# Kernel tuning notes

Hardware: AMD Instinct MI355X
Metric: run time of the kernel (lower is better)

The kernel has to match this reference:

```python
import jax, jax.numpy as jnp
import numpy as np

N = 30000   # fluid particles
E = 480000  # edges
F = 4       # fluidFeatures (in channels)
P = 8       # RBF basis size per dim (dims=[8], 1D)
LAYERS = [32, 64, 64, 2]


def hat_basis(x, n):
    # 'linear' RBF: hat functions on n evenly spaced centers in [-1, 1]
    centers = jnp.linspace(-1.0, 1.0, n, dtype=x.dtype)
    spacing = 2.0 / (n - 1)
    return jnp.maximum(0.0, 1.0 - jnp.abs(x[:, None] - centers[None, :]) / spacing)  # [E, n]


def rbf_conv(x, fi, fj, d, W, b, mask, n_nodes):
    # x: [N, Cin]; d: [E, 1] clamped; W: [P, Cin, Cout]; b: [Cout]
    phi = hat_basis(d[:, 0], W.shape[0])      # [E, P]
    xj = x[fj]                                 # gather source features [E, Cin]
    msg = jnp.zeros((xj.shape[0], W.shape[2]), dtype=x.dtype)
    for p in range(W.shape[0]):                # small fixed P=8 loop keeps memory O(E*Cout)
        msg = msg + phi[:, p, None] * (xj @ W[p])
    msg = jnp.where(mask[:, None], msg, 0.0)   # centerIgnore: drop self edges fi==fj
    out = jax.ops.segment_sum(msg, fi, num_segments=n_nodes)  # scatter-reduce to targets
    return out + b


def _xavier(key, shape_in, shape_out):
    lim = float(np.sqrt(6.0 / (shape_in + shape_out)))
    return jax.random.uniform(key, (shape_in, shape_out), jnp.float32, -lim, lim)


def setup_inputs() -> dict:
    key = jax.random.key(0)
    ks = jax.random.split(key, 16)
    fluidFeatures = jax.random.normal(ks[0], (N, F), jnp.float32)
    fi = jax.random.randint(ks[1], (E,), 0, N)
    fj = jax.random.randint(ks[2], (E,), 0, N)
    distances = jax.random.normal(ks[3], (E, 1), jnp.float32)
    # conv channels: 4->32, 64->64, 64->64, 64->2
    cio = [(F, 32), (2 * 32, 64), (64, 64), (64, 2)]
    inp = {"fluidFeatures": fluidFeatures, "fi": fi, "fj": fj, "distances": distances}
    for li, (ci, co) in enumerate(cio):
        inp[f"cW{li}"] = jax.random.normal(ks[4 + li], (P, ci, co), jnp.float32) * (1.0 / np.sqrt(P * ci))
        inp[f"cb{li}"] = jnp.zeros((co,), jnp.float32)
        inp[f"fW{li}"] = _xavier(ks[8 + li], ci, co)   # stored [in, out]
        inp[f"fb{li}"] = jnp.zeros((co,), jnp.float32)
    return inp


def reference(fluidFeatures, fi, fj, distances,
              cW0, cb0, fW0, fb0, cW1, cb1, fW1, fb1,
              cW2, cb2, fW2, fb2, cW3, cb3, fW3, fb3):
    n_nodes = fluidFeatures.shape[0]
    mask = fi != fj                     # centerIgnore (mask instead of filter: jit-safe)
    d = jnp.clip(distances, -1.0, 1.0)

    conv0 = rbf_conv(fluidFeatures, fi, fj, d, cW0, cb0, mask, n_nodes)  # [N, 32]
    lin0 = fluidFeatures @ fW0 + fb0                                      # [N, 32]
    ans = jnp.concatenate([lin0, conv0], axis=1)                          # [N, 64]

    # i = 1: features[0]=32 != features[1]=64 -> no residual
    ansc = jax.nn.relu(ans)
    ans = rbf_conv(ansc, fi, fj, d, cW1, cb1, mask, n_nodes) + (ansc @ fW1 + fb1)
    # i = 2: features[1]==features[2]==64 and shapes match -> residual
    ansc = jax.nn.relu(ans)
    ans = rbf_conv(ansc, fi, fj, d, cW2, cb2, mask, n_nodes) + (ansc @ fW2 + fb2) + ans
    # i = 3: 64 -> 2, no residual
    ansc = jax.nn.relu(ans)
    ans = rbf_conv(ansc, fi, fj, d, cW3, cb3, mask, n_nodes) + (ansc @ fW3 + fb3)

    return ans  # dim == 1 (dims=[8]) -> no /128
```

## Files before the change

kernel.cpp:

```cpp
#include <hip/hip_runtime.h>


#define CAP 48

typedef __attribute__((ext_vector_type(8))) short short8;
typedef __attribute__((ext_vector_type(4))) float f32x4;
typedef int v4i __attribute__((ext_vector_type(4)));

__device__ __forceinline__ short bf16s(float f) {
  unsigned u = __float_as_uint(f);
  return (short)((u + 0x7FFF + ((u >> 16) & 1)) >> 16);
}
__device__ __forceinline__ float b2f(unsigned short s) {
  return __uint_as_float(((unsigned)s) << 16);
}
__device__ __forceinline__ unsigned pack2(float a, float b) {
  return (unsigned)(unsigned short)bf16s(a) | ((unsigned)(unsigned short)bf16s(b) << 16);
}
__device__ __forceinline__ float dec_w0(int v) {
  return __uint_as_float(0x3F800000u | (((unsigned)v & 0xFFFu) << 11)) - 1.0f;
}
__device__ __forceinline__ float dec_sf(int v) {
  return (float)(((unsigned)v >> 12) & 1u);
}
__device__ __forceinline__ unsigned long long rfl64(unsigned long long x) {
  unsigned lo = __builtin_amdgcn_readfirstlane((unsigned)x);
  unsigned hi = __builtin_amdgcn_readfirstlane((unsigned)(x >> 32));
  return ((unsigned long long)hi << 32) | (unsigned long long)lo;
}

#define LOAD_RECS32Q(JROW, CPTR, MRAW)                                      \
  v4i q0, q1, q2, q3, q4, q5, q6, q7;                                       \
  int MRAW;                                                                 \
  asm volatile("s_load_dwordx4 %0, %9, 0x0\n\t"                             \
               "s_load_dwordx4 %1, %9, 0x10\n\t"                            \
               "s_load_dwordx4 %2, %9, 0x20\n\t"                            \
               "s_load_dwordx4 %3, %9, 0x30\n\t"                            \
               "s_load_dwordx4 %4, %9, 0x40\n\t"                            \
               "s_load_dwordx4 %5, %9, 0x50\n\t"                            \
               "s_load_dwordx4 %6, %9, 0x60\n\t"                            \
               "s_load_dwordx4 %7, %9, 0x70\n\t"                            \
               "s_load_dword %8, %10, 0x0\n\t"                              \
               "s_waitcnt lgkmcnt(0)"                                       \
               : "=&s"(q0), "=&s"(q1), "=&s"(q2), "=&s"(q3), "=&s"(q4),     \
                 "=&s"(q5), "=&s"(q6), "=&s"(q7), "=&s"(MRAW)               \
               : "s"(JROW), "s"(CPTR)                                       \
               : "memory")

#define LOAD_RECS16TQ(JROW)                                                 \
  v4i qt0, qt1, qt2, qt3;                                                   \
  asm volatile("s_load_dwordx4 %0, %4, 0x80\n\t"                            \
               "s_load_dwordx4 %1, %4, 0x90\n\t"                            \
               "s_load_dwordx4 %2, %4, 0xA0\n\t"                            \
               "s_load_dwordx4 %3, %4, 0xB0\n\t"                            \
               "s_waitcnt lgkmcnt(0)"                                       \
               : "=&s"(qt0), "=&s"(qt1), "=&s"(qt2), "=&s"(qt3)             \
               : "s"(JROW)                                                  \
               : "memory")

#define RECK(K) ((K) < 4 ? q0[(K) & 3] : (K) < 8 ? q1[(K) & 3] :            \
                 (K) < 12 ? q2[(K) & 3] : (K) < 16 ? q3[(K) & 3] :          \
                 (K) < 20 ? q4[(K) & 3] : (K) < 24 ? q5[(K) & 3] :          \
                 (K) < 28 ? q6[(K) & 3] : q7[(K) & 3])
#define RECT(K) ((K) < 4 ? qt0[(K) & 3] : (K) < 8 ? qt1[(K) & 3] :          \
                 (K) < 12 ? qt2[(K) & 3] : qt3[(K) & 3])

__global__ void fill_prep(const float* __restrict__ dist,
                          const int* __restrict__ fi, const int* __restrict__ fj,
                          int* __restrict__ cnt, int* __restrict__ jw, int nE,
                          const float* __restrict__ cW0, const float* __restrict__ fW0,
                          const float* __restrict__ cb0, const float* __restrict__ fb0,
                          const float* __restrict__ cW1, const float* __restrict__ fW1,
                          const float* __restrict__ cb1, const float* __restrict__ fb1,
                          const float* __restrict__ cW2, const float* __restrict__ fW2,
                          const float* __restrict__ cb2, const float* __restrict__ fb2,
                          const float* __restrict__ cW3,
                          short* __restrict__ W0T, short* __restrict__ W1T,
                          short* __restrict__ W2T, short* __restrict__ WT3,
                          float* __restrict__ BIA,
                          const float* __restrict__ X,
                          unsigned short* __restrict__ Xb, int n,
                          int fillBlocks, int prepBlocks) {
  if ((int)blockIdx.x < fillBlocks) {
    int e = blockIdx.x * blockDim.x + threadIdx.x;
    if (e >= nE) return;
    int i = fi[e], j = fj[e];
    if (i == j) return;
    float d = fminf(1.0f, fmaxf(-1.0f, dist[e]));
    float u = (d + 1.0f) * 3.5f;
    int p = min((int)u, 6);
    float w0 = 1.0f - (u - (float)p);
    int wq = min((int)(w0 * 4096.0f + 0.5f), 4095);
    int pos = atomicAdd(&cnt[i], 1);
    if (pos < CAP)
      jw[(size_t)i * CAP + pos] =
          (int)(((unsigned)j << 17) | ((unsigned)p << 14) | 0x1000u | (unsigned)wq);
  } else if ((int)blockIdx.x < fillBlocks + prepBlocks) {
    int idx = ((int)blockIdx.x - fillBlocks) * blockDim.x + threadIdx.x;
    if (idx < 36864) {
      int o = idx / 576, k = idx - o * 576;
      float v = (k < 512) ? cW1[((size_t)(k >> 6) * 64 + (k & 63)) * 64 + o]
                          : fW1[(size_t)(k - 512) * 64 + o];
      W1T[idx] = bf16s(v);
    } else if (idx < 73728) {
      int r = idx - 36864;
      int o = r / 576, k = r - o * 576;
      float v = (k < 512) ? cW2[((size_t)(k >> 6) * 64 + (k & 63)) * 64 + o]
                          : fW2[(size_t)(k - 512) * 64 + o];
      W2T[r] = bf16s(v);
    } else if (idx < 110592) {
      int r = idx - 73728;
      int o = r / 576, k = r - o * 576;
      float v = 0.0f;
      if (k < 512) {
        int s = k >> 6, ci = k & 63;
        if (ci < 4 && o >= 32) v = cW0[((size_t)s * 4 + ci) * 32 + (o - 32)];
      } else {
        int c = k - 512;
        if (c < 4 && o < 32) v = fW0[(size_t)c * 32 + o];
      }
      W0T[r] = bf16s(v);
    } else if (idx < 111616) {
      int r = idx - 110592;
      int t = r >> 6, ch = r & 63;
      WT3[r] = bf16s(cW3[((size_t)(t >> 1) * 64 + ch) * 2 + (t & 1)]);
    } else if (idx < 111808) {
      int r = idx - 111616;
      int layer = r >> 6, ch = r & 63;
      float v;
      if (layer == 0) v = (ch < 32) ? fb0[ch] : cb0[ch - 32];
      else if (layer == 1) v = cb1[ch] + fb1[ch];
      else v = cb2[ch] + fb2[ch];
      BIA[r] = v;
    }
  } else {
    int idx = ((int)blockIdx.x - fillBlocks - prepBlocks) * blockDim.x + threadIdx.x;
    if (idx >= n * 64) return;
    int i = idx >> 6, c = idx & 63;
    float v = (c < 4) ? X[(size_t)i * 4 + c] : 0.0f;
    Xb[idx] = (unsigned short)bf16s(v);
  }
}

__global__ __launch_bounds__(1024, 8) void conv_agg(
    const unsigned short* __restrict__ prev,
    const int* __restrict__ cnt, const int* __restrict__ jw,
    const short* __restrict__ WTn,
    const float* __restrict__ bias,
    const float* __restrict__ resid,
    float* __restrict__ outF32,
    unsigned short* __restrict__ outAnsc,
    const short* __restrict__ WT3,
    float* __restrict__ T, int flags, int n) {
  __shared__ __align__(16) unsigned short sA[16 * 584];
  __shared__ __align__(16) unsigned short sC[16 * 72];
  const int tid = threadIdx.x;
  const int w = tid >> 6;
  const int lane = tid & 63;
  const int half = lane >> 5;
  const int l32 = lane & 31;
  const unsigned ln4 = (unsigned)l32 * 4u;
  const int nodeBase = blockIdx.x * 16;
  const int i = nodeBase + w;
  const bool valid = (i < n);
  const int ic = valid ? i : 0;
  const int* jrow = (const int*)rfl64((unsigned long long)(jw + (size_t)ic * CAP));
  const int* cptr = (const int*)rfl64((unsigned long long)(cnt + ic));
  LOAD_RECS32Q(jrow, cptr, mraw);
  const int m = valid ? min(mraw, CAP) : 0;
  const unsigned short own = prev[(size_t)ic * 64 + lane];
  float aL0 = 0, aL1 = 0, aL2 = 0, aL3 = 0, aL4 = 0, aL5 = 0, aL6 = 0, aL7 = 0;
  float aH0 = 0, aH1 = 0, aH2 = 0, aH3 = 0, aH4 = 0, aH5 = 0, aH6 = 0, aH7 = 0;
  unsigned u0, u1, u2, u3, u4, u5, u6, u7;
  int v0, v1, v2, v3, v4, v5, v6, v7;
#define GSET(G, EA, EB)                                                     \
  { v##G = half ? (EB) : (EA);                                              \
    u##G = ((((unsigned)v##G) >> 10) & 0xFFFFFF80u) + ln4; }
#define GISSUE8(BASE)                                                       \
  asm volatile("global_load_dword %0, %0, %[bb]\n\t"                        \
               "global_load_dword %1, %1, %[bb]\n\t"                        \
               "global_load_dword %2, %2, %[bb]\n\t"                        \
               "global_load_dword %3, %3, %[bb]\n\t"                        \
               "global_load_dword %4, %4, %[bb]\n\t"                        \
               "global_load_dword %5, %5, %[bb]\n\t"                        \
               "global_load_dword %6, %6, %[bb]\n\t"                        \
               "global_load_dword %7, %7, %[bb]\n\t"                        \
               "s_waitcnt vmcnt(0)"                                         \
               : "+v"(u0), "+v"(u1), "+v"(u2), "+v"(u3),                    \
                 "+v"(u4), "+v"(u5), "+v"(u6), "+v"(u7)                     \
               : [bb] "s"(BASE)                                             \
               : "memory")
#define SLOT1(S)                                                            \
  { float sel_ = (p_ == (S)) ? w0_ : (p_ == ((S)-1)) ? w1_ : 0.0f;          \
    aL##S = fmaf(sel_, xl_, aL##S);                                         \
    aH##S = fmaf(sel_, xh_, aH##S); }
#define GCONS(G)                                                            \
  { int vv_ = v##G;                                                         \
    unsigned uu_ = u##G;                                                    \
    float w0_ = dec_w0(vv_);                                                \
    float w1_ = dec_sf(vv_) - w0_;                                          \
    int p_ = (int)(((unsigned)vv_ >> 14) & 7u);                             \
    float xl_ = __uint_as_float(uu_ << 16);                                 \
    float xh_ = __uint_as_float(uu_ & 0xFFFF0000u);                         \
    SLOT1(0) SLOT1(1) SLOT1(2) SLOT1(3) SLOT1(4) SLOT1(5) SLOT1(6) SLOT1(7) }
  GSET(0, RECK(0), RECK(1))   GSET(1, RECK(2), RECK(3))
  GSET(2, RECK(4), RECK(5))   GSET(3, RECK(6), RECK(7))
  GSET(4, RECK(8), RECK(9))   GSET(5, RECK(10), RECK(11))
  GSET(6, RECK(12), RECK(13)) GSET(7, RECK(14), RECK(15))
  GISSUE8(prev);
  GCONS(0) GCONS(1) GCONS(2) GCONS(3) GCONS(4) GCONS(5) GCONS(6) GCONS(7)
  if (m > 16) {
    GSET(0, RECK(16), RECK(17)) GSET(1, RECK(18), RECK(19))
    GSET(2, RECK(20), RECK(21)) GSET(3, RECK(22), RECK(23))
    GSET(4, RECK(24), RECK(25)) GSET(5, RECK(26), RECK(27))
    GSET(6, RECK(28), RECK(29)) GSET(7, RECK(30), RECK(31))
    GISSUE8(prev);
    GCONS(0) GCONS(1) GCONS(2) GCONS(3) GCONS(4) GCONS(5) GCONS(6) GCONS(7)
    if (m > 32) {
      LOAD_RECS16TQ(jrow);
      GSET(0, RECT(0), RECT(1))   GSET(1, RECT(2), RECT(3))
      GSET(2, RECT(4), RECT(5))   GSET(3, RECT(6), RECT(7))
      GSET(4, RECT(8), RECT(9))   GSET(5, RECT(10), RECT(11))
      GSET(6, RECT(12), RECT(13)) GSET(7, RECT(14), RECT(15))
      GISSUE8(prev);
      GCONS(0) GCONS(1) GCONS(2) GCONS(3) GCONS(4) GCONS(5) GCONS(6) GCONS(7)
    }
  }
#undef GSET
#undef GISSUE8
#undef SLOT1
#undef GCONS
#define RED(S)                                                              \
  aL##S += __shfl_xor(aL##S, 32, 64);                                       \
  aH##S += __shfl_xor(aH##S, 32, 64);
  RED(0) RED(1) RED(2) RED(3) RED(4) RED(5) RED(6) RED(7)
#undef RED
  unsigned short* sAr = sA + w * 584;
  if (half == 0) {
#define SWR(S) ((unsigned*)(sAr + (S)*64))[l32] = pack2(aL##S, aH##S);
    SWR(0) SWR(1) SWR(2) SWR(3) SWR(4) SWR(5) SWR(6) SWR(7)
#undef SWR
  }
  sAr[512 + lane] = own;
  __syncthreads();

  if (w < 4) {
    const int mrow = lane & 15, quad = lane >> 4, t = w;
    const unsigned rowoff = (unsigned)((t * 16 + mrow) * 1152 + quad * 16);
    const unsigned short* brow = sA + mrow * 584 + quad * 8;
    f32x4 acc4 = {0, 0, 0, 0};
    short8 f0, f1, f2, f3, f4, f5;
#define WLOAD6(CO)                                                          \
  asm volatile("global_load_dwordx4 %0, %[vo], %[bb] offset:0\n\t"          \
               "global_load_dwordx4 %1, %[vo], %[bb] offset:64\n\t"         \
               "global_load_dwordx4 %2, %[vo], %[bb] offset:128\n\t"        \
               "global_load_dwordx4 %3, %[vo], %[bb] offset:192\n\t"        \
               "global_load_dwordx4 %4, %[vo], %[bb] offset:256\n\t"        \
               "global_load_dwordx4 %5, %[vo], %[bb] offset:320\n\t"        \
               "s_waitcnt vmcnt(0)"                                         \
               : "=&v"(f0), "=&v"(f1), "=&v"(f2), "=&v"(f3),                \
                 "=&v"(f4), "=&v"(f5)                                       \
               : [vo] "v"(rowoff + (CO)), [bb] "s"(WTn)                     \
               : "memory")
#define MM6(KK0)                                                            \
  acc4 = __builtin_amdgcn_mfma_f32_16x16x32_bf16(                           \
      f0, *(const short8*)(brow + ((KK0) + 0) * 32), acc4, 0, 0, 0);        \
  acc4 = __builtin_amdgcn_mfma_f32_16x16x32_bf16(                           \
      f1, *(const short8*)(brow + ((KK0) + 1) * 32), acc4, 0, 0, 0);        \
  acc4 = __builtin_amdgcn_mfma_f32_16x16x32_bf16(                           \
      f2, *(const short8*)(brow + ((KK0) + 2) * 32), acc4, 0, 0, 0);        \
  acc4 = __builtin_amdgcn_mfma_f32_16x16x32_bf16(                           \
      f3, *(const short8*)(brow + ((KK0) + 3) * 32), acc4, 0, 0, 0);        \
  acc4 = __builtin_amdgcn_mfma_f32_16x16x32_bf16(                           \
      f4, *(const short8*)(brow + ((KK0) + 4) * 32), acc4, 0, 0, 0);        \
  acc4 = __builtin_amdgcn_mfma_f32_16x16x32_bf16(                           \
      f5, *(const short8*)(brow + ((KK0) + 5) * 32), acc4, 0, 0, 0);
    WLOAD6(0);    MM6(0);
    WLOAD6(384);  MM6(6);
    WLOAD6(768);  MM6(12);
#undef WLOAD6
#undef MM6
    const int node2 = nodeBase + mrow;
    const int ch0 = t * 16 + quad * 4;
    if (node2 < n) {
      float4 bb4 = *(const float4*)(bias + ch0);
      float4 rv = make_float4(0.f, 0.f, 0.f, 0.f);
      if (flags & 1) rv = *(const float4*)(resid + (size_t)node2 * 64 + ch0);
      float o0 = acc4[0] + bb4.x + rv.x;
      float o1 = acc4[1] + bb4.y + rv.y;
      float o2 = acc4[2] + bb4.z + rv.z;
      float o3 = acc4[3] + bb4.w + rv.w;
      if (flags & 2) {
        *(float2*)(outF32 + (size_t)node2 * 64 + ch0) = make_float2(o0, o1);
        *(float2*)(outF32 + (size_t)node2 * 64 + ch0 + 2) = make_float2(o2, o3);
      }
      unsigned lo = pack2(fmaxf(o0, 0.f), fmaxf(o1, 0.f));
      unsigned hi = pack2(fmaxf(o2, 0.f), fmaxf(o3, 0.f));
      *(uint2*)(outAnsc + (size_t)node2 * 64 + ch0) = make_uint2(lo, hi);
      if (flags & 4) {
        *(unsigned*)(sC + mrow * 72 + ch0) = lo;
        *(unsigned*)(sC + mrow * 72 + ch0 + 2) = hi;
      }
    } else if (flags & 4) {
      *(unsigned*)(sC + mrow * 72 + ch0) = 0u;
      *(unsigned*)(sC + mrow * 72 + ch0 + 2) = 0u;
    }
  }
  if (flags & 4) {
    __syncthreads();
    if (w == 0) {
      const int mrow = lane & 15, quad = lane >> 4;
      short8 b0 = *(const short8*)(sC + mrow * 72 + quad * 8);
      short8 b1 = *(const short8*)(sC + mrow * 72 + quad * 8 + 32);
      short8 a0v = *(const short8*)(WT3 + mrow * 64 + quad * 8);
      short8 a1v = *(const short8*)(WT3 + mrow * 64 + quad * 8 + 32);
      f32x4 acc4 = {0, 0, 0, 0};
      acc4 = __builtin_amdgcn_mfma_f32_16x16x32_bf16(a0v, b0, acc4, 0, 0, 0);
      acc4 = __builtin_amdgcn_mfma_f32_16x16x32_bf16(a1v, b1, acc4, 0, 0, 0);
      const int node2 = nodeBase + mrow;
      if (node2 < n) {
        float* tr = T + (size_t)node2 * 18 + quad * 4;
        *(float2*)(tr) = make_float2(acc4[0], acc4[1]);
        *(float2*)(tr + 2) = make_float2(acc4[2], acc4[3]);
      }
    }
  }
}

__global__ __launch_bounds__(256, 4) void layer3_kernel(
    const unsigned short* __restrict__ Xb,
    const float* __restrict__ T,
    const int* __restrict__ cnt, const int* __restrict__ jw,
    const float* __restrict__ cb3, const float* __restrict__ fb3,
    const float* __restrict__ fW3,
    float* __restrict__ out, int n) {
  const int lane = threadIdx.x & 63;
  const int i = (blockIdx.x * blockDim.x + threadIdx.x) >> 6;
  if (i >= n) return;
  const int m = min(cnt[i], CAP);
  float c0 = 0.0f, c1 = 0.0f;
  if (lane < m) {
    int v = jw[(size_t)i * CAP + lane];
    unsigned j = (unsigned)v >> 17;
    unsigned p = ((unsigned)v >> 14) & 7u;
    unsigned off9 = j * 9u + p;
    float w0 = dec_w0(v);
    float w1 = 1.0f - w0;
    const float* tb = T + (size_t)off9 * 2;
    float2 ta = *(const float2*)(tb);
    float2 tc = *(const float2*)(tb + 2);
    c0 = w0 * ta.x + w1 * tc.x;
    c1 = w0 * ta.y + w1 * tc.y;
  }
  float xi = b2f(Xb[(size_t)i * 64 + lane]);
  float2 fw = *(const float2*)(fW3 + lane * 2);
  c0 = fmaf(xi, fw.x, c0);
  c1 = fmaf(xi, fw.y, c1);
  #pragma unroll
  for (int off = 32; off > 0; off >>= 1) {
    c0 += __shfl_xor(c0, off, 64);
    c1 += __shfl_xor(c1, off, 64);
  }
  if (lane == 0) {
    out[(size_t)i * 2 + 0] = c0 + cb3[0] + fb3[0];
    out[(size_t)i * 2 + 1] = c1 + cb3[1] + fb3[1];
  }
}

extern "C" void kernel_launch(void* const* d_in, const int* in_sizes, int n_in,
                              void* d_out, int out_size, void* d_ws, size_t ws_size,
                              hipStream_t stream) {
  const float* X    = (const float*)d_in[0];
  const int*   fi   = (const int*)d_in[1];
  const int*   fj   = (const int*)d_in[2];
  const float* dist = (const float*)d_in[3];
  const float* cW0 = (const float*)d_in[4];  const float* cb0 = (const float*)d_in[5];
  const float* fW0 = (const float*)d_in[6];  const float* fb0 = (const float*)d_in[7];
  const float* cW1 = (const float*)d_in[8];  const float* cb1 = (const float*)d_in[9];
  const float* fW1 = (const float*)d_in[10]; const float* fb1 = (const float*)d_in[11];
  const float* cW2 = (const float*)d_in[12]; const float* cb2 = (const float*)d_in[13];
  const float* fW2 = (const float*)d_in[14]; const float* fb2 = (const float*)d_in[15];
  const float* cW3 = (const float*)d_in[16]; const float* cb3 = (const float*)d_in[17];
  const float* fW3 = (const float*)d_in[18]; const float* fb3 = (const float*)d_in[19];
  float* out = (float*)d_out;

  const int n  = in_sizes[0] / 4;
  const int nE = in_sizes[1];

  unsigned short* ansc0 = (unsigned short*)d_ws;
  float*          ans1  = (float*)(ansc0 + (size_t)n * 64);
  unsigned short* ansc1 = (unsigned short*)(ans1 + (size_t)n * 64);
  unsigned short* ansc2 = ansc1 + (size_t)n * 64;
  float*          T     = (float*)(ansc2 + (size_t)n * 64);
  unsigned short* Xb16  = (unsigned short*)(T + (size_t)n * 18);
  short* W1T = (short*)(Xb16 + (size_t)n * 64);
  short* W2T = W1T + 36864;
  short* W0T = W2T + 36864;
  short* WT3 = W0T + 36864;
  float* BIA = (float*)(WT3 + 1024);
  int*   jw  = (int*)(BIA + 192);
  int*   cnt = jw + (size_t)n * CAP;

  hipMemsetAsync(jw, 0, ((size_t)n * CAP + n) * sizeof(int), stream);
  const int fillBlocks = (nE + 255) / 256;
  const int prepBlocks = (111808 + 255) / 256;
  const int xbBlocks   = (n * 64 + 255) / 256;
  fill_prep<<<fillBlocks + prepBlocks + xbBlocks, 256, 0, stream>>>(
      dist, fi, fj, cnt, jw, nE,
      cW0, fW0, cb0, fb0, cW1, fW1, cb1, fb1, cW2, fW2, cb2, fb2, cW3,
      W0T, W1T, W2T, WT3, BIA, X, Xb16, n, fillBlocks, prepBlocks);

  const int nodeBlocks = (n + 15) / 16;
  conv_agg<<<nodeBlocks, 1024, 0, stream>>>(Xb16, cnt, jw, W0T, BIA,
                                            ans1, ans1, ansc0, WT3, T, 0, n);
  conv_agg<<<nodeBlocks, 1024, 0, stream>>>(ansc0, cnt, jw, W1T, BIA + 64,
                                            ans1, ans1, ansc1, WT3, T, 2, n);
  conv_agg<<<nodeBlocks, 1024, 0, stream>>>(ansc1, cnt, jw, W2T, BIA + 128,
                                            ans1, ans1, ansc2, WT3, T, 5, n);
  layer3_kernel<<<(n * 64 + 255) / 256, 256, 0, stream>>>(ansc2, T, cnt, jw,
                                                          cb3, fb3, fW3, out, n);
}
```

Before: 258.9 us.

## Gather one channel per lane with ushort loads and switch-based basis scatter

The edge-gather loop in conv_agg now has each of the 64 lanes load one bf16 channel per neighbor with global_load_ushort, instead of two channels per lane split across wave halves. This removes the cross-half shuffle reduction and the pack step. The per-slot select-and-FMA chain over all 8 basis slots becomes a switch that updates only the two active slots. Sixteen loads are issued per batch with a partial vmcnt wait so the first eight can be consumed while the rest are in flight. The input bf16 conversion in fill_prep also writes 16-byte vectors. In exchange the kernel issues more, smaller memory instructions, and the switch may diverge within a wave.

```diff
diff --git a/kernel.cpp b/kernel.cpp
--- a/kernel.cpp
+++ b/kernel.cpp
@@ -135,10 +135,15 @@
     }
   } else {
     int idx = ((int)blockIdx.x - fillBlocks - prepBlocks) * blockDim.x + threadIdx.x;
-    if (idx >= n * 64) return;
-    int i = idx >> 6, c = idx & 63;
-    float v = (c < 4) ? X[(size_t)i * 4 + c] : 0.0f;
-    Xb[idx] = (unsigned short)bf16s(v);
+    if (idx >= n * 8) return;
+    int i = idx >> 3, g = idx & 7;
+    uint4 val = make_uint4(0u, 0u, 0u, 0u);
+    if (g == 0) {
+      float4 x = *(const float4*)(X + (size_t)i * 4);
+      val.x = pack2(x.x, x.y);
+      val.y = pack2(x.z, x.w);
+    }
+    *(uint4*)(Xb + (size_t)i * 64 + g * 8) = val;
   }
 }
 
@@ -157,9 +162,7 @@
   const int tid = threadIdx.x;
   const int w = tid >> 6;
   const int lane = tid & 63;
-  const int half = lane >> 5;
-  const int l32 = lane & 31;
-  const unsigned ln4 = (unsigned)l32 * 4u;
+  const unsigned ln2 = (unsigned)lane * 2u;
   const int nodeBase = blockIdx.x * 16;
   const int i = nodeBase + w;
   const bool valid = (i < n);
@@ -169,79 +172,108 @@
   LOAD_RECS32Q(jrow, cptr, mraw);
   const int m = valid ? min(mraw, CAP) : 0;
   const unsigned short own = prev[(size_t)ic * 64 + lane];
-  float aL0 = 0, aL1 = 0, aL2 = 0, aL3 = 0, aL4 = 0, aL5 = 0, aL6 = 0, aL7 = 0;
-  float aH0 = 0, aH1 = 0, aH2 = 0, aH3 = 0, aH4 = 0, aH5 = 0, aH6 = 0, aH7 = 0;
+  float aS0 = 0, aS1 = 0, aS2 = 0, aS3 = 0, aS4 = 0, aS5 = 0, aS6 = 0, aS7 = 0;
   unsigned u0, u1, u2, u3, u4, u5, u6, u7;
-  int v0, v1, v2, v3, v4, v5, v6, v7;
-#define GSET(G, EA, EB)                                                     \
-  { v##G = half ? (EB) : (EA);                                              \
-    u##G = ((((unsigned)v##G) >> 10) & 0xFFFFFF80u) + ln4; }
-#define GISSUE8(BASE)                                                       \
-  asm volatile("global_load_dword %0, %0, %[bb]\n\t"                        \
-               "global_load_dword %1, %1, %[bb]\n\t"                        \
-               "global_load_dword %2, %2, %[bb]\n\t"                        \
-               "global_load_dword %3, %3, %[bb]\n\t"                        \
-               "global_load_dword %4, %4, %[bb]\n\t"                        \
-               "global_load_dword %5, %5, %[bb]\n\t"                        \
-               "global_load_dword %6, %6, %[bb]\n\t"                        \
-               "global_load_dword %7, %7, %[bb]\n\t"                        \
-               "s_waitcnt vmcnt(0)"                                         \
+  unsigned u8, u9, u10, u11, u12, u13, u14, u15;
+#define GSETU(G, V) { int v_ = (V);                                         \
+    u##G = ((((unsigned)v_) >> 10) & 0xFFFFFF80u) + ln2; }
+#define GISSUE16_W8(BASE)                                                   \
+  asm volatile("global_load_ushort %0, %0, %[bb]\n\t"                       \
+               "global_load_ushort %1, %1, %[bb]\n\t"                       \
+               "global_load_ushort %2, %2, %[bb]\n\t"                       \
+               "global_load_ushort %3, %3, %[bb]\n\t"                       \
+               "global_load_ushort %4, %4, %[bb]\n\t"                       \
+               "global_load_ushort %5, %5, %[bb]\n\t"                       \
+               "global_load_ushort %6, %6, %[bb]\n\t"                       \
+               "global_load_ushort %7, %7, %[bb]\n\t"                       \
+               "global_load_ushort %8, %8, %[bb]\n\t"                       \
+               "global_load_ushort %9, %9, %[bb]\n\t"                       \
+               "global_load_ushort %10, %10, %[bb]\n\t"                     \
+               "global_load_ushort %11, %11, %[bb]\n\t"                     \
+               "global_load_ushort %12, %12, %[bb]\n\t"                     \
+               "global_load_ushort %13, %13, %[bb]\n\t"                     \
+               "global_load_ushort %14, %14, %[bb]\n\t"                     \
+               "global_load_ushort %15, %15, %[bb]\n\t"                     \
+               "s_waitcnt vmcnt(8)"                                         \
                : "+v"(u0), "+v"(u1), "+v"(u2), "+v"(u3),                    \
-                 "+v"(u4), "+v"(u5), "+v"(u6), "+v"(u7)                     \
+                 "+v"(u4), "+v"(u5), "+v"(u6), "+v"(u7),                    \
+                 "+v"(u8), "+v"(u9), "+v"(u10), "+v"(u11),                  \
+                 "+v"(u12), "+v"(u13), "+v"(u14), "+v"(u15)                 \
                : [bb] "s"(BASE)                                             \
                : "memory")
-#define SLOT1(S)                                                            \
-  { float sel_ = (p_ == (S)) ? w0_ : (p_ == ((S)-1)) ? w1_ : 0.0f;          \
-    aL##S = fmaf(sel_, xl_, aL##S);                                         \
-    aH##S = fmaf(sel_, xh_, aH##S); }
-#define GCONS(G)                                                            \
-  { int vv_ = v##G;                                                         \
-    unsigned uu_ = u##G;                                                    \
-    float w0_ = dec_w0(vv_);                                                \
-    float w1_ = dec_sf(vv_) - w0_;                                          \
-    int p_ = (int)(((unsigned)vv_ >> 14) & 7u);                             \
-    float xl_ = __uint_as_float(uu_ << 16);                                 \
-    float xh_ = __uint_as_float(uu_ & 0xFFFF0000u);                         \
-    SLOT1(0) SLOT1(1) SLOT1(2) SLOT1(3) SLOT1(4) SLOT1(5) SLOT1(6) SLOT1(7) }
-  GSET(0, RECK(0), RECK(1))   GSET(1, RECK(2), RECK(3))
-  GSET(2, RECK(4), RECK(5))   GSET(3, RECK(6), RECK(7))
-  GSET(4, RECK(8), RECK(9))   GSET(5, RECK(10), RECK(11))
-  GSET(6, RECK(12), RECK(13)) GSET(7, RECK(14), RECK(15))
-  GISSUE8(prev);
-  GCONS(0) GCONS(1) GCONS(2) GCONS(3) GCONS(4) GCONS(5) GCONS(6) GCONS(7)
+#define WAITV0_HI                                                           \
+  asm volatile("s_waitcnt vmcnt(0)"                                         \
+               : "+v"(u8), "+v"(u9), "+v"(u10), "+v"(u11),                  \
+                 "+v"(u12), "+v"(u13), "+v"(u14), "+v"(u15)                 \
+               :: "memory")
+#define GCONSU(G, V) { int v_ = (V);                                        \
+    float w0_ = dec_w0(v_);                                                 \
+    float w1_ = dec_sf(v_) - w0_;                                           \
+    float xv_ = __uint_as_float(u##G << 16);                                \
+    switch ((((unsigned)v_) >> 14) & 7u) {                                  \
+      case 0: aS0 = fmaf(w0_, xv_, aS0); aS1 = fmaf(w1_, xv_, aS1); break;  \
+      case 1: aS1 = fmaf(w0_, xv_, aS1); aS2 = fmaf(w1_, xv_, aS2); break;  \
+      case 2: aS2 = fmaf(w0_, xv_, aS2); aS3 = fmaf(w1_, xv_, aS3); break;  \
+      case 3: aS3 = fmaf(w0_, xv_, aS3); aS4 = fmaf(w1_, xv_, aS4); break;  \
+      case 4: aS4 = fmaf(w0_, xv_, aS4); aS5 = fmaf(w1_, xv_, aS5); break;  \
+      case 5: aS5 = fmaf(w0_, xv_, aS5); aS6 = fmaf(w1_, xv_, aS6); break;  \
+      case 6: aS6 = fmaf(w0_, xv_, aS6); aS7 = fmaf(w1_, xv_, aS7); break;  \
+      default: break;                                                       \
+    } }
+  GSETU(0, RECK(0))   GSETU(1, RECK(1))   GSETU(2, RECK(2))   GSETU(3, RECK(3))
+  GSETU(4, RECK(4))   GSETU(5, RECK(5))   GSETU(6, RECK(6))   GSETU(7, RECK(7))
+  GSETU(8, RECK(8))   GSETU(9, RECK(9))   GSETU(10, RECK(10)) GSETU(11, RECK(11))
+  GSETU(12, RECK(12)) GSETU(13, RECK(13)) GSETU(14, RECK(14)) GSETU(15, RECK(15))
+  GISSUE16_W8(prev);
+  GCONSU(0, RECK(0)) GCONSU(1, RECK(1)) GCONSU(2, RECK(2)) GCONSU(3, RECK(3))
+  GCONSU(4, RECK(4)) GCONSU(5, RECK(5)) GCONSU(6, RECK(6)) GCONSU(7, RECK(7))
+  WAITV0_HI;
+  GCONSU(8, RECK(8))   GCONSU(9, RECK(9))   GCONSU(10, RECK(10))
+  GCONSU(11, RECK(11)) GCONSU(12, RECK(12)) GCONSU(13, RECK(13))
+  GCONSU(14, RECK(14)) GCONSU(15, RECK(15))
   if (m > 16) {
-    GSET(0, RECK(16), RECK(17)) GSET(1, RECK(18), RECK(19))
-    GSET(2, RECK(20), RECK(21)) GSET(3, RECK(22), RECK(23))
-    GSET(4, RECK(24), RECK(25)) GSET(5, RECK(26), RECK(27))
-    GSET(6, RECK(28), RECK(29)) GSET(7, RECK(30), RECK(31))
-    GISSUE8(prev);
-    GCONS(0) GCONS(1) GCONS(2) GCONS(3) GCONS(4) GCONS(5) GCONS(6) GCONS(7)
+    GSETU(0, RECK(16))  GSETU(1, RECK(17))  GSETU(2, RECK(18))  GSETU(3, RECK(19))
+    GSETU(4, RECK(20))  GSETU(5, RECK(21))  GSETU(6, RECK(22))  GSETU(7, RECK(23))
+    GSETU(8, RECK(24))  GSETU(9, RECK(25))  GSETU(10, RECK(26)) GSETU(11, RECK(27))
+    GSETU(12, RECK(28)) GSETU(13, RECK(29)) GSETU(14, RECK(30)) GSETU(15, RECK(31))
+    GISSUE16_W8(prev);
+    GCONSU(0, RECK(16)) GCONSU(1, RECK(17)) GCONSU(2, RECK(18)) GCONSU(3, RECK(19))
+    GCONSU(4, RECK(20)) GCONSU(5, RECK(21)) GCONSU(6, RECK(22)) GCONSU(7, RECK(23))
+    WAITV0_HI;
+    GCONSU(8, RECK(24))  GCONSU(9, RECK(25))  GCONSU(10, RECK(26))
+    GCONSU(11, RECK(27)) GCONSU(12, RECK(28)) GCONSU(13, RECK(29))
+    GCONSU(14, RECK(30)) GCONSU(15, RECK(31))
     if (m > 32) {
       LOAD_RECS16TQ(jrow);
-      GSET(0, RECT(0), RECT(1))   GSET(1, RECT(2), RECT(3))
-      GSET(2, RECT(4), RECT(5))   GSET(3, RECT(6), RECT(7))
-      GSET(4, RECT(8), RECT(9))   GSET(5, RECT(10), RECT(11))
-      GSET(6, RECT(12), RECT(13)) GSET(7, RECT(14), RECT(15))
-      GISSUE8(prev);
-      GCONS(0) GCONS(1) GCONS(2) GCONS(3) GCONS(4) GCONS(5) GCONS(6) GCONS(7)
+      GSETU(0, RECT(0))   GSETU(1, RECT(1))   GSETU(2, RECT(2))   GSETU(3, RECT(3))
+      GSETU(4, RECT(4))   GSETU(5, RECT(5))   GSETU(6, RECT(6))   GSETU(7, RECT(7))
+      GSETU(8, RECT(8))   GSETU(9, RECT(9))   GSETU(10, RECT(10)) GSETU(11, RECT(11))
+      GSETU(12, RECT(12)) GSETU(13, RECT(13)) GSETU(14, RECT(14)) GSETU(15, RECT(15))
+      GISSUE16_W8(prev);
+      GCONSU(0, RECT(0)) GCONSU(1, RECT(1)) GCONSU(2, RECT(2)) GCONSU(3, RECT(3))
+      GCONSU(4, RECT(4)) GCONSU(5, RECT(5)) GCONSU(6, RECT(6)) GCONSU(7, RECT(7))
+      WAITV0_HI;
+      GCONSU(8, RECT(8))   GCONSU(9, RECT(9))   GCONSU(10, RECT(10))
+      GCONSU(11, RECT(11)) GCONSU(12, RECT(12)) GCONSU(13, RECT(13))
+      GCONSU(14, RECT(14)) GCONSU(15, RECT(15))
     }
   }
-#undef GSET
-#undef GISSUE8
-#undef SLOT1
-#undef GCONS
-#define RED(S)                                                              \
-  aL##S += __shfl_xor(aL##S, 32, 64);                                       \
-  aH##S += __shfl_xor(aH##S, 32, 64);
-  RED(0) RED(1) RED(2) RED(3) RED(4) RED(5) RED(6) RED(7)
-#undef RED
-  unsigned short* sAr = sA + w * 584;
-  if (half == 0) {
-#define SWR(S) ((unsigned*)(sAr + (S)*64))[l32] = pack2(aL##S, aH##S);
-    SWR(0) SWR(1) SWR(2) SWR(3) SWR(4) SWR(5) SWR(6) SWR(7)
-#undef SWR
-  }
-  sAr[512 + lane] = own;
+#undef GSETU
+#undef GISSUE16_W8
+#undef WAITV0_HI
+#undef GCONSU
+  {
+    unsigned short* sAr = sA + w * 584;
+    sAr[0 * 64 + lane] = (unsigned short)bf16s(aS0);
+    sAr[1 * 64 + lane] = (unsigned short)bf16s(aS1);
+    sAr[2 * 64 + lane] = (unsigned short)bf16s(aS2);
+    sAr[3 * 64 + lane] = (unsigned short)bf16s(aS3);
+    sAr[4 * 64 + lane] = (unsigned short)bf16s(aS4);
+    sAr[5 * 64 + lane] = (unsigned short)bf16s(aS5);
+    sAr[6 * 64 + lane] = (unsigned short)bf16s(aS6);
+    sAr[7 * 64 + lane] = (unsigned short)bf16s(aS7);
+    sAr[512 + lane] = own;
+  }
   __syncthreads();
 
   if (w < 4) {
@@ -404,7 +436,7 @@
   hipMemsetAsync(jw, 0, ((size_t)n * CAP + n) * sizeof(int), stream);
   const int fillBlocks = (nE + 255) / 256;
   const int prepBlocks = (111808 + 255) / 256;
-  const int xbBlocks   = (n * 64 + 255) / 256;
+  const int xbBlocks   = (n * 8 + 255) / 256;
   fill_prep<<<fillBlocks + prepBlocks + xbBlocks, 256, 0, stream>>>(
       dist, fi, fj, cnt, jw, nE,
       cW0, fW0, cb0, fb0, cW1, fW1, cb1, fb1, cW2, fW2, cb2, fb2, cW3,
```

Measured after the change: 249.4 us. 3.7% less time.
